# Kernel tuning notes

Measured on AMD Instinct MI355X. Metric: run time of the kernel, lower is better.

The kernel has to match this reference:

```python
import jax, jax.numpy as jnp
import numpy as np

NUM_EXPERT = 16
IN_FEAT = 1024
OUT_FEAT = 2048
N_TOKENS = 4096


def setup_inputs() -> dict:
    key = jax.random.key(0)
    k1, k2, k3 = jax.random.split(key, 3)
    x = jax.random.uniform(k1, (N_TOKENS, IN_FEAT), dtype=jnp.float32)
    gate = jax.random.randint(k2, (N_TOKENS,), 0, NUM_EXPERT, dtype=jnp.int32)
    # expert weights: [num_expert, out_feat, in_feat]
    weight = jax.random.normal(k3, (NUM_EXPERT, OUT_FEAT, IN_FEAT), dtype=jnp.float32) * 0.02
    return {"x": x, "gate": gate, "weight": weight}


def reference(x, gate, weight):
    # out[b] = weight[gate[b]] @ x[b]
    # Avoid materializing weight[gate] ([B, O, I] would be huge): scan over the
    # small, fixed expert axis with input masking (tokens not routed to expert e
    # contribute zero rows to that expert's GEMM).
    B = x.shape[0]
    E, O, I = weight.shape
    out0 = jnp.zeros((B, O), dtype=x.dtype)

    def body(out, ew):
        e, W = ew  # W: [O, I]
        xm = jnp.where((gate == e)[:, None], x, 0.0)  # [B, I] masked tokens
        return out + jnp.einsum("bi,oi->bo", xm, W), None

    out, _ = jax.lax.scan(body, out0, (jnp.arange(E), weight))
    return out
```

## Files before the change

kernel.cpp:

```cpp
#include <hip/hip_runtime.h>
#include <hip/hip_bf16.h>
#include <stdint.h>

#define N_TOKENS   4096
#define IN_FEAT    1024
#define OUT_FEAT   2048
#define NUM_EXPERT 16

#define BM 128
#define BK 32
#define NT (IN_FEAT / BK)
#define BNW 128
#define GROWS 512
#define MAX_ROWS  6144

typedef __bf16 bf16x8 __attribute__((ext_vector_type(8)));
typedef float  f32x4  __attribute__((ext_vector_type(4)));
typedef unsigned short us8 __attribute__((ext_vector_type(8)));

__device__ __forceinline__ unsigned short f32_to_bf16_rne(float f) {
  union { float f; uint32_t u; } v; v.f = f;
  uint32_t u = v.u;
  u += 0x7fffu + ((u >> 16) & 1u);
  return (unsigned short)(u >> 16);
}

__device__ __forceinline__ void async_copy16(const void* g, void* l) {
  __builtin_amdgcn_global_load_lds(
      (const __attribute__((address_space(1))) unsigned int*)g,
      (__attribute__((address_space(3))) unsigned int*)l, 16, 0, 0);
}

__global__ void k_setup(const int* __restrict__ gate,
                        int* __restrict__ pstart,
                        int* __restrict__ row_token)
{
  __shared__ int cnt[NUM_EXPERT];
  __shared__ int cur[NUM_EXPERT];
  __shared__ int ps[NUM_EXPERT];
  const int tid = threadIdx.x;
  if (tid < NUM_EXPERT) { cnt[tid] = 0; cur[tid] = 0; }
  __syncthreads();
  for (int b = tid; b < N_TOKENS; b += 256) atomicAdd(&cnt[gate[b]], 1);
  for (int r = tid; r < MAX_ROWS; r += 256) row_token[r] = -1;
  __syncthreads();
  if (tid == 0) {
    int p = 0;
    for (int e = 0; e < NUM_EXPERT; ++e) {
      ps[e] = p; pstart[e] = p;
      p += ((cnt[e] + BM - 1) / BM) * BM;
    }
    pstart[NUM_EXPERT] = p;
  }
  __syncthreads();
  for (int b = tid; b < N_TOKENS; b += 256) {
    int e = gate[b];
    int pos = atomicAdd(&cur[e], 1);
    row_token[ps[e] + pos] = b;
  }
}

__global__ void k_gather_x(const float4* __restrict__ x,
                           const int* __restrict__ row_token,
                           us8* __restrict__ xs) {
  const int r = blockIdx.x * 2 + (threadIdx.x >> 7);
  const int c = threadIdx.x & 127;
  const int tok = row_token[r];
  us8 o;
  if (tok >= 0) {
    float4 a = x[tok * 256 + c * 2];
    float4 b = x[tok * 256 + c * 2 + 1];
    o[0] = f32_to_bf16_rne(a.x); o[1] = f32_to_bf16_rne(a.y);
    o[2] = f32_to_bf16_rne(a.z); o[3] = f32_to_bf16_rne(a.w);
    o[4] = f32_to_bf16_rne(b.x); o[5] = f32_to_bf16_rne(b.y);
    o[6] = f32_to_bf16_rne(b.z); o[7] = f32_to_bf16_rne(b.w);
  } else {
    o = (us8)0;
  }
  xs[r * 128 + c] = o;
}

__global__ void __launch_bounds__(512, 2)
k_gemm(const unsigned short* __restrict__ xs,
       const float* __restrict__ w,
       const int* __restrict__ pstart,
       const int* __restrict__ row_token,
       float* __restrict__ out) {
  __shared__ f32x4 Bs[2][1024];
  __shared__ int rowtok_s[GROWS];

  const int e    = blockIdx.x;
  const int nwin = blockIdx.y * BNW;
  const int seg0 = pstart[e];
  const int seg_len = pstart[e + 1] - seg0;
  if (seg_len <= 0) return;

  const int tid  = threadIdx.x;
  const int wid  = tid >> 6;
  const int lane = tid & 63;
  const int lr   = lane & 15;
  const int quad = lane >> 4;

  const int rB = tid >> 3;
  const int cB = (tid & 7) ^ (rB & 7);
  const float* bgp = w + (size_t)e * OUT_FEAT * IN_FEAT
                       + (size_t)(nwin + rB) * IN_FEAT + cB * 4;

  auto stageB = [&](int t, int b) {
    const int k0 = t * BK;
    async_copy16(bgp + k0,                Bs[b] +       wid * 64);
    async_copy16(bgp + 64 * IN_FEAT + k0, Bs[b] + 512 + wid * 64);
  };

  const int nGroups = (seg_len + GROWS - 1) / GROWS;

  for (int g = 0; g < nGroups; ++g) {
    __syncthreads();

    {
      const int grow = g * GROWS + tid;
      rowtok_s[tid] = (grow < seg_len) ? row_token[seg0 + grow] : -1;
    }

    const unsigned short* apm[4];
#pragma unroll
    for (int mi = 0; mi < 4; ++mi) {
      const int grow = g * GROWS + wid * 64 + mi * 16 + lr;
      const int arow = (grow < seg_len) ? grow : 0;
      apm[mi] = xs + (size_t)(seg0 + arow) * IN_FEAT + quad * 8;
    }

    auto loadA = [&](int t, bf16x8* dst) {
#pragma unroll
      for (int mi = 0; mi < 4; ++mi)
        dst[mi] = *(const bf16x8*)(apm[mi] + t * BK);
    };

    f32x4 acc[4][8];
    const f32x4 z = {0.f, 0.f, 0.f, 0.f};
#pragma unroll
    for (int i = 0; i < 4; ++i)
#pragma unroll
      for (int j = 0; j < 8; ++j) acc[i][j] = z;

    bf16x8 afA[4], afB[4];

    stageB(0, 0);
    loadA(0, afA);

    asm volatile("s_waitcnt lgkmcnt(0)" ::: "memory");
    __builtin_amdgcn_s_barrier();

    auto step = [&](int t, bf16x8* afc, bf16x8* afn) {
      const int buf = t & 1;
      if (t + 1 < NT) {
        stageB(t + 1, buf ^ 1);
        loadA(t + 1, afn);
        asm volatile("s_waitcnt vmcnt(6)" ::: "memory");
      } else {
        asm volatile("s_waitcnt vmcnt(0)" ::: "memory");
      }
      __builtin_amdgcn_s_barrier();
      asm volatile("" ::: "memory");

      bf16x8 bf[8];
#pragma unroll
      for (int ni = 0; ni < 8; ++ni) {
        const int n = ni * 16 + lr;
        f32x4 c0 = Bs[buf][n * 8 + ((2 * quad)     ^ (n & 7))];
        f32x4 c1 = Bs[buf][n * 8 + ((2 * quad + 1) ^ (n & 7))];
        bf16x8 b;
        b[0] = (__bf16)c0[0]; b[1] = (__bf16)c0[1];
        b[2] = (__bf16)c0[2]; b[3] = (__bf16)c0[3];
        b[4] = (__bf16)c1[0]; b[5] = (__bf16)c1[1];
        b[6] = (__bf16)c1[2]; b[7] = (__bf16)c1[3];
        bf[ni] = b;
      }
#pragma unroll
      for (int mi = 0; mi < 4; ++mi)
#pragma unroll
        for (int ni = 0; ni < 8; ++ni)
          acc[mi][ni] = __builtin_amdgcn_mfma_f32_16x16x32_bf16(
              afc[mi], bf[ni], acc[mi][ni], 0, 0, 0);

      asm volatile("" ::: "memory");
      __builtin_amdgcn_s_barrier();
    };

    for (int t = 0; t < NT; t += 2) {
      step(t,     afA, afB);
      step(t + 1, afB, afA);
    }

#pragma unroll
    for (int mi = 0; mi < 4; ++mi) {
      const int mb = wid * 64 + mi * 16 + quad * 4;
      const int t0 = rowtok_s[mb + 0];
      const int t1 = rowtok_s[mb + 1];
      const int t2 = rowtok_s[mb + 2];
      const int t3 = rowtok_s[mb + 3];
#pragma unroll
      for (int ni = 0; ni < 8; ++ni) {
        const int n = nwin + ni * 16 + lr;
        f32x4 c = acc[mi][ni];
        if (t0 >= 0) out[(size_t)t0 * OUT_FEAT + n] = c[0];
        if (t1 >= 0) out[(size_t)t1 * OUT_FEAT + n] = c[1];
        if (t2 >= 0) out[(size_t)t2 * OUT_FEAT + n] = c[2];
        if (t3 >= 0) out[(size_t)t3 * OUT_FEAT + n] = c[3];
      }
    }
  }
}

extern "C" void kernel_launch(void* const* d_in, const int* in_sizes, int n_in,
                              void* d_out, int out_size, void* d_ws, size_t ws_size,
                              hipStream_t stream) {
  const float* x    = (const float*)d_in[0];
  const int*   gate = (const int*)d_in[1];
  const float* w    = (const float*)d_in[2];
  float* out = (float*)d_out;

  char* ws = (char*)d_ws;
  unsigned short* xs = (unsigned short*)ws;
  int* row_token = (int*)(ws + 12582912);
  int* pstart = row_token + MAX_ROWS;

  k_setup<<<1, 256, 0, stream>>>(gate, pstart, row_token);
  k_gather_x<<<MAX_ROWS / 2, 256, 0, stream>>>((const float4*)x, row_token,
                                               (us8*)xs);
  dim3 g(NUM_EXPERT, OUT_FEAT / BNW);
  k_gemm<<<g, 512, 0, stream>>>(xs, w, pstart, row_token, out);
}
```

Baseline: 260.4 us.

## Fuse routing and fp32 gather into the grouped GEMM kernel

Drops the separate setup and gather/convert kernels. Each GEMM block now scans the gate array itself to build its expert's token list in shared memory, reads fp32 x rows directly from global memory, and converts them to bf16 in registers. The aim is to remove two kernel launches and the round trip through the bf16 staging buffer. In exchange, every block repeats the gate scan with shared atomics, and the A-operand traffic doubles because fp32 is loaded and converted in the inner loop, which needs more registers and more loads in flight.

```diff
diff --git a/kernel.cpp b/kernel.cpp
--- a/kernel.cpp
+++ b/kernel.cpp
@@ -7,23 +7,13 @@
 #define OUT_FEAT   2048
 #define NUM_EXPERT 16
 
-#define BM 128
 #define BK 32
 #define NT (IN_FEAT / BK)
 #define BNW 128
 #define GROWS 512
-#define MAX_ROWS  6144
 
 typedef __bf16 bf16x8 __attribute__((ext_vector_type(8)));
 typedef float  f32x4  __attribute__((ext_vector_type(4)));
-typedef unsigned short us8 __attribute__((ext_vector_type(8)));
-
-__device__ __forceinline__ unsigned short f32_to_bf16_rne(float f) {
-  union { float f; uint32_t u; } v; v.f = f;
-  uint32_t u = v.u;
-  u += 0x7fffu + ((u >> 16) & 1u);
-  return (unsigned short)(u >> 16);
-}
 
 __device__ __forceinline__ void async_copy16(const void* g, void* l) {
   __builtin_amdgcn_global_load_lds(
@@ -31,69 +21,17 @@
       (__attribute__((address_space(3))) unsigned int*)l, 16, 0, 0);
 }
 
-__global__ void k_setup(const int* __restrict__ gate,
-                        int* __restrict__ pstart,
-                        int* __restrict__ row_token)
-{
-  __shared__ int cnt[NUM_EXPERT];
-  __shared__ int cur[NUM_EXPERT];
-  __shared__ int ps[NUM_EXPERT];
-  const int tid = threadIdx.x;
-  if (tid < NUM_EXPERT) { cnt[tid] = 0; cur[tid] = 0; }
-  __syncthreads();
-  for (int b = tid; b < N_TOKENS; b += 256) atomicAdd(&cnt[gate[b]], 1);
-  for (int r = tid; r < MAX_ROWS; r += 256) row_token[r] = -1;
-  __syncthreads();
-  if (tid == 0) {
-    int p = 0;
-    for (int e = 0; e < NUM_EXPERT; ++e) {
-      ps[e] = p; pstart[e] = p;
-      p += ((cnt[e] + BM - 1) / BM) * BM;
-    }
-    pstart[NUM_EXPERT] = p;
-  }
-  __syncthreads();
-  for (int b = tid; b < N_TOKENS; b += 256) {
-    int e = gate[b];
-    int pos = atomicAdd(&cur[e], 1);
-    row_token[ps[e] + pos] = b;
-  }
-}
-
-__global__ void k_gather_x(const float4* __restrict__ x,
-                           const int* __restrict__ row_token,
-                           us8* __restrict__ xs) {
-  const int r = blockIdx.x * 2 + (threadIdx.x >> 7);
-  const int c = threadIdx.x & 127;
-  const int tok = row_token[r];
-  us8 o;
-  if (tok >= 0) {
-    float4 a = x[tok * 256 + c * 2];
-    float4 b = x[tok * 256 + c * 2 + 1];
-    o[0] = f32_to_bf16_rne(a.x); o[1] = f32_to_bf16_rne(a.y);
-    o[2] = f32_to_bf16_rne(a.z); o[3] = f32_to_bf16_rne(a.w);
-    o[4] = f32_to_bf16_rne(b.x); o[5] = f32_to_bf16_rne(b.y);
-    o[6] = f32_to_bf16_rne(b.z); o[7] = f32_to_bf16_rne(b.w);
-  } else {
-    o = (us8)0;
-  }
-  xs[r * 128 + c] = o;
-}
-
 __global__ void __launch_bounds__(512, 2)
-k_gemm(const unsigned short* __restrict__ xs,
-       const float* __restrict__ w,
-       const int* __restrict__ pstart,
-       const int* __restrict__ row_token,
-       float* __restrict__ out) {
+k_moe(const float* __restrict__ x,
+      const int* __restrict__ gate,
+      const float* __restrict__ w,
+      float* __restrict__ out) {
   __shared__ f32x4 Bs[2][1024];
-  __shared__ int rowtok_s[GROWS];
+  __shared__ unsigned short toks[N_TOKENS];
+  __shared__ int cnt_s;
 
   const int e    = blockIdx.x;
   const int nwin = blockIdx.y * BNW;
-  const int seg0 = pstart[e];
-  const int seg_len = pstart[e + 1] - seg0;
-  if (seg_len <= 0) return;
 
   const int tid  = threadIdx.x;
   const int wid  = tid >> 6;
@@ -112,28 +50,42 @@
     async_copy16(bgp + 64 * IN_FEAT + k0, Bs[b] + 512 + wid * 64);
   };
 
-  const int nGroups = (seg_len + GROWS - 1) / GROWS;
+  stageB(0, 0);
 
-  for (int g = 0; g < nGroups; ++g) {
-    __syncthreads();
+  if (tid == 0) cnt_s = 0;
+  __syncthreads();
+  for (int b = tid; b < N_TOKENS; b += 512) {
+    if (gate[b] == e) {
+      int p = atomicAdd(&cnt_s, 1);
+      toks[p] = (unsigned short)b;
+    }
+  }
+  __syncthreads();
+  const int cnt = cnt_s;
+  if (cnt == 0) {
+    asm volatile("s_waitcnt vmcnt(0)" ::: "memory");
+    return;
+  }
 
-    {
-      const int grow = g * GROWS + tid;
-      rowtok_s[tid] = (grow < seg_len) ? row_token[seg0 + grow] : -1;
+  const int nG = (cnt + GROWS - 1) / GROWS;
+
+  for (int g = 0; g < nG; ++g) {
+    if (g > 0) stageB(0, 0);
+
+    const float* ap[4];
+#pragma unroll
+    for (int mi = 0; mi < 4; ++mi) {
+      const int s = g * GROWS + wid * 64 + mi * 16 + lr;
+      const int tk = (s < cnt) ? (int)toks[s] : (int)toks[0];
+      ap[mi] = x + (size_t)tk * IN_FEAT + quad * 8;
     }
 
-    const unsigned short* apm[4];
+    auto loadAraw = [&](int t, f32x4* dst) {
 #pragma unroll
-    for (int mi = 0; mi < 4; ++mi) {
-      const int grow = g * GROWS + wid * 64 + mi * 16 + lr;
-      const int arow = (grow < seg_len) ? grow : 0;
-      apm[mi] = xs + (size_t)(seg0 + arow) * IN_FEAT + quad * 8;
-    }
-
-    auto loadA = [&](int t, bf16x8* dst) {
-#pragma unroll
-      for (int mi = 0; mi < 4; ++mi)
-        dst[mi] = *(const bf16x8*)(apm[mi] + t * BK);
+      for (int mi = 0; mi < 4; ++mi) {
+        dst[mi * 2]     = *(const f32x4*)(ap[mi] + t * BK);
+        dst[mi * 2 + 1] = *(const f32x4*)(ap[mi] + t * BK + 4);
+      }
     };
 
     f32x4 acc[4][8];
@@ -143,25 +95,33 @@
 #pragma unroll
       for (int j = 0; j < 8; ++j) acc[i][j] = z;
 
-    bf16x8 afA[4], afB[4];
+    f32x4 rawA[8], rawB[8];
+    loadAraw(0, rawA);
 
-    stageB(0, 0);
-    loadA(0, afA);
-
-    asm volatile("s_waitcnt lgkmcnt(0)" ::: "memory");
-    __builtin_amdgcn_s_barrier();
-
-    auto step = [&](int t, bf16x8* afc, bf16x8* afn) {
+    auto step = [&](int t, const f32x4* rawc, f32x4* rawn) {
       const int buf = t & 1;
       if (t + 1 < NT) {
         stageB(t + 1, buf ^ 1);
-        loadA(t + 1, afn);
-        asm volatile("s_waitcnt vmcnt(6)" ::: "memory");
+        loadAraw(t + 1, rawn);
+        asm volatile("s_waitcnt vmcnt(10)" ::: "memory");
       } else {
         asm volatile("s_waitcnt vmcnt(0)" ::: "memory");
       }
       __builtin_amdgcn_s_barrier();
       asm volatile("" ::: "memory");
+
+      bf16x8 af[4];
+#pragma unroll
+      for (int mi = 0; mi < 4; ++mi) {
+        const f32x4 a0 = rawc[mi * 2];
+        const f32x4 a1 = rawc[mi * 2 + 1];
+        bf16x8 a;
+        a[0] = (__bf16)a0[0]; a[1] = (__bf16)a0[1];
+        a[2] = (__bf16)a0[2]; a[3] = (__bf16)a0[3];
+        a[4] = (__bf16)a1[0]; a[5] = (__bf16)a1[1];
+        a[6] = (__bf16)a1[2]; a[7] = (__bf16)a1[3];
+        af[mi] = a;
+      }
 
       bf16x8 bf[8];
 #pragma unroll
@@ -181,32 +141,28 @@
 #pragma unroll
         for (int ni = 0; ni < 8; ++ni)
           acc[mi][ni] = __builtin_amdgcn_mfma_f32_16x16x32_bf16(
-              afc[mi], bf[ni], acc[mi][ni], 0, 0, 0);
+              af[mi], bf[ni], acc[mi][ni], 0, 0, 0);
 
       asm volatile("" ::: "memory");
       __builtin_amdgcn_s_barrier();
     };
 
     for (int t = 0; t < NT; t += 2) {
-      step(t,     afA, afB);
-      step(t + 1, afB, afA);
+      step(t,     rawA, rawB);
+      step(t + 1, rawB, rawA);
     }
 
 #pragma unroll
     for (int mi = 0; mi < 4; ++mi) {
-      const int mb = wid * 64 + mi * 16 + quad * 4;
-      const int t0 = rowtok_s[mb + 0];
-      const int t1 = rowtok_s[mb + 1];
-      const int t2 = rowtok_s[mb + 2];
-      const int t3 = rowtok_s[mb + 3];
+      const int mb = g * GROWS + wid * 64 + mi * 16 + quad * 4;
 #pragma unroll
       for (int ni = 0; ni < 8; ++ni) {
         const int n = nwin + ni * 16 + lr;
         f32x4 c = acc[mi][ni];
-        if (t0 >= 0) out[(size_t)t0 * OUT_FEAT + n] = c[0];
-        if (t1 >= 0) out[(size_t)t1 * OUT_FEAT + n] = c[1];
-        if (t2 >= 0) out[(size_t)t2 * OUT_FEAT + n] = c[2];
-        if (t3 >= 0) out[(size_t)t3 * OUT_FEAT + n] = c[3];
+        if (mb + 0 < cnt) out[(size_t)toks[mb + 0] * OUT_FEAT + n] = c[0];
+        if (mb + 1 < cnt) out[(size_t)toks[mb + 1] * OUT_FEAT + n] = c[1];
+        if (mb + 2 < cnt) out[(size_t)toks[mb + 2] * OUT_FEAT + n] = c[2];
+        if (mb + 3 < cnt) out[(size_t)toks[mb + 3] * OUT_FEAT + n] = c[3];
       }
     }
   }
@@ -220,14 +176,6 @@
   const float* w    = (const float*)d_in[2];
   float* out = (float*)d_out;
 
-  char* ws = (char*)d_ws;
-  unsigned short* xs = (unsigned short*)ws;
-  int* row_token = (int*)(ws + 12582912);
-  int* pstart = row_token + MAX_ROWS;
-
-  k_setup<<<1, 256, 0, stream>>>(gate, pstart, row_token);
-  k_gather_x<<<MAX_ROWS / 2, 256, 0, stream>>>((const float4*)x, row_token,
-                                               (us8*)xs);
   dim3 g(NUM_EXPERT, OUT_FEAT / BNW);
-  k_gemm<<<g, 512, 0, stream>>>(xs, w, pstart, row_token, out);
+  k_moe<<<g, 512, 0, stream>>>(x, gate, w, out);
 }
```

Measured after the change: 269.8 us. 3.6% more time.
